# Optimization experiments

Measured on AMD Instinct MI355X. Metric: run time of the kernel, lower is better.

## Reference

```python
import jax, jax.numpy as jnp
import numpy as np
import math

B, SQ, SK, HEADS, DH = 4, 4096, 308, 8, 64
INNER = HEADS * DH


def setup_inputs() -> dict:
    key = jax.random.key(0)
    k1, k2, k3, k4, k5 = jax.random.split(key, 5)
    q = jax.random.normal(k1, (B, SQ, INNER), dtype=jnp.float32)
    k = jax.random.normal(k2, (B, SK, INNER), dtype=jnp.float32)
    v = jax.random.normal(k3, (B, SK, INNER), dtype=jnp.float32)
    # mask_scale: positive multiplicative rescale (H*W / mask_area in original)
    mask_scale = jax.random.uniform(k4, (B, HEADS, SQ, SK), dtype=jnp.float32) + 0.5
    # mask_bool: region membership mask (masks > 0.5 in original)
    mask_bool = jax.random.randint(k5, (B, HEADS, SQ, SK), 0, 2) > 0
    return {"q": q, "k": k, "v": v, "mask_scale": mask_scale,
            "mask_bool": mask_bool, "heads": HEADS}


def reference(q, k, v, mask_scale, mask_bool, heads):
    b, sq, inner = q.shape
    dh = inner // heads
    # (b, s, h*dh) -> (b, h, s, dh)
    def split_heads(t):
        return t.reshape(b, -1, heads, dh).transpose(0, 2, 1, 3)
    qh, kh, vh = split_heads(q), split_heads(k), split_heads(v)
    scores = jnp.einsum('bhqd,bhkd->bhqk', qh, kh) / math.sqrt(dh)
    scores = scores * mask_scale
    scores = jnp.where(mask_bool, scores, -jnp.inf)
    attn = jax.nn.softmax(scores, axis=-1)
    out = jnp.einsum('bhqk,bhkd->bhqd', attn, vh)
    # (b, h, q, dh) -> (b, q, h*dh)
    return out.transpose(0, 2, 1, 3).reshape(b, sq, heads * dh)
```

## Files before the change

### kernel.cpp

```cpp
#include <hip/hip_runtime.h>


#define NB     4
#define NSQ    4096
#define NSK    308
#define NH     8
#define NDH    64
#define NINNER 512
#define NKT    20
#define QTILE  128
#define NTHREADS 512
#define PF     4
#define LDS_BYTES ((NKT*2*64*8 + NKT*4*64*4) * 2)

typedef _Float16 h8 __attribute__((ext_vector_type(8)));
typedef _Float16 h4 __attribute__((ext_vector_type(4)));
typedef float    f4 __attribute__((ext_vector_type(4)));
typedef int      i4 __attribute__((ext_vector_type(4)));

__global__ __launch_bounds__(NTHREADS) void omost_attn(
    const float* __restrict__ Qg, const float* __restrict__ Kg,
    const float* __restrict__ Vg, const float* __restrict__ MSg,
    const int*   __restrict__ MBg, float* __restrict__ Og)
{
  extern __shared__ __align__(16) _Float16 smem[];
  _Float16* Klds = smem;
  _Float16* Vlds = smem + NKT*2*64*8;

  const int tid  = threadIdx.x;
  const int lane = tid & 63;
  const int wv   = tid >> 6;
  const int lg   = lane >> 4;
  const int lr   = lane & 15;

  const int wg = blockIdx.x;
  const int qt = wg & (NSQ / QTILE - 1);
  const int bh = wg >> 5;
  const int b  = bh >> 3;
  const int h  = bh & 7;

  const int q0   = qt * QTILE + wv * 16;
  const int qrow = q0 + lr;
  const size_t mrow = ((size_t)bh * NSQ + qrow) * NSK;

  f4 msb[PF];
  i4 mbb[PF];
  #pragma unroll
  for (int d = 0; d < PF; ++d) {
    int kb = d * 16 + lg * 4;
    msb[d] = *(const f4*)(MSg + mrow + kb);
    mbb[d] = *(const i4*)(MBg + mrow + kb);
  }

  const float* Kb = Kg + (size_t)b * NSK * NINNER + h * NDH;
  #pragma unroll
  for (int i = 0; i < (NKT*2*64) / NTHREADS; ++i) {
    int s   = tid + i * NTHREADS;
    int l   = s & 63;
    int dhc = (s >> 6) & 1;
    int kt  = s >> 7;
    int row = kt * 16 + (l & 15);
    int col = dhc * 32 + ((l >> 4) << 3);
    h8 hk;
    #pragma unroll
    for (int j = 0; j < 8; ++j) hk[j] = (_Float16)0.f;
    if (row < NSK) {
      const float* p = Kb + (size_t)row * NINNER + col;
      f4 a = *(const f4*)p;
      f4 c = *(const f4*)(p + 4);
      hk[0]=(_Float16)a[0]; hk[1]=(_Float16)a[1]; hk[2]=(_Float16)a[2]; hk[3]=(_Float16)a[3];
      hk[4]=(_Float16)c[0]; hk[5]=(_Float16)c[1]; hk[6]=(_Float16)c[2]; hk[7]=(_Float16)c[3];
    }
    *(h8*)(Klds + (size_t)s * 8) = hk;
  }

  const float* Vb = Vg + (size_t)b * NSK * NINNER + h * NDH;
  #pragma unroll
  for (int i = 0; i < (NKT*4*64) / NTHREADS; ++i) {
    int s    = tid + i * NTHREADS;
    int l    = s & 63;
    int nt   = (s >> 6) & 3;
    int kt   = s >> 8;
    int col  = nt * 16 + (l & 15);
    int row0 = kt * 16 + ((l >> 4) << 2);
    h4 hv;
    #pragma unroll
    for (int j = 0; j < 4; ++j) hv[j] = (_Float16)0.f;
    #pragma unroll
    for (int j = 0; j < 4; ++j) {
      int row = row0 + j;
      if (row < NSK) hv[j] = (_Float16)Vb[(size_t)row * NINNER + col];
    }
    *(h4*)(Vlds + (size_t)s * 4) = hv;
  }
  __syncthreads();

  const float NEG_INF = -__builtin_inff();

  const float* Qb = Qg + ((size_t)b * NSQ + qrow) * NINNER + h * NDH;
  h8 qf[2];
  #pragma unroll
  for (int dhc = 0; dhc < 2; ++dhc) {
    const float* p = Qb + dhc * 32 + lg * 8;
    f4 a = *(const f4*)p;
    f4 c = *(const f4*)(p + 4);
    h8 t;
    t[0]=(_Float16)a[0]; t[1]=(_Float16)a[1]; t[2]=(_Float16)a[2]; t[3]=(_Float16)a[3];
    t[4]=(_Float16)c[0]; t[5]=(_Float16)c[1]; t[6]=(_Float16)c[2]; t[7]=(_Float16)c[3];
    qf[dhc] = t;
  }

  f4 S[NKT];
  float rmax = NEG_INF;
  const h8* Kf = (const h8*)Klds;
  #pragma unroll
  for (int kt = 0; kt < NKT; ++kt) {
    f4 ms = msb[kt % PF];
    i4 mb = mbb[kt % PF];
    if (kt + PF < NKT) {
      int kb  = (kt + PF) * 16 + lg * 4;
      int kbl = kb > (NSK - 4) ? (NSK - 4) : kb;
      msb[(kt + PF) % PF] = *(const f4*)(MSg + mrow + kbl);
      mbb[(kt + PF) % PF] = *(const i4*)(MBg + mrow + kbl);
    }
    f4 c = {0.f, 0.f, 0.f, 0.f};
    c = __builtin_amdgcn_mfma_f32_16x16x32_f16(Kf[(kt*2+0)*64 + lane], qf[0], c, 0, 0, 0);
    c = __builtin_amdgcn_mfma_f32_16x16x32_f16(Kf[(kt*2+1)*64 + lane], qf[1], c, 0, 0, 0);

    const int kb0 = kt * 16 + lg * 4;
    f4 s;
    #pragma unroll
    for (int r = 0; r < 4; ++r) {
      bool ok = (kb0 + r < NSK) && (mb[r] != 0);
      s[r] = ok ? c[r] * 0.125f * ms[r] : NEG_INF;
      rmax = fmaxf(rmax, s[r]);
    }
    S[kt] = s;
  }

  rmax = fmaxf(rmax, __shfl_xor(rmax, 16, 64));
  rmax = fmaxf(rmax, __shfl_xor(rmax, 32, 64));
  float ssum = 0.f;
  #pragma unroll
  for (int kt = 0; kt < NKT; ++kt) {
    f4 s = S[kt];
    #pragma unroll
    for (int r = 0; r < 4; ++r) { float p = __expf(s[r] - rmax); s[r] = p; ssum += p; }
    S[kt] = s;
  }
  ssum += __shfl_xor(ssum, 16, 64);
  ssum += __shfl_xor(ssum, 32, 64);
  const float inv = 1.f / ssum;

  f4 acc[4];
  #pragma unroll
  for (int nt = 0; nt < 4; ++nt) acc[nt] = (f4){0.f, 0.f, 0.f, 0.f};
  const h4* Vf = (const h4*)Vlds;
  #pragma unroll
  for (int kt = 0; kt < NKT; ++kt) {
    h4 pa;
    #pragma unroll
    for (int r = 0; r < 4; ++r) pa[r] = (_Float16)(S[kt][r] * inv);
    #pragma unroll
    for (int nt = 0; nt < 4; ++nt)
      acc[nt] = __builtin_amdgcn_mfma_f32_16x16x16f16(pa, Vf[(kt*4+nt)*64 + lane], acc[nt], 0, 0, 0);
  }

  float* Ob = Og + (size_t)b * NSQ * NINNER + h * NDH;
  #pragma unroll
  for (int nt = 0; nt < 4; ++nt) {
    #pragma unroll
    for (int r = 0; r < 4; ++r) {
      int qq = q0 + lg * 4 + r;
      Ob[(size_t)qq * NINNER + nt * 16 + lr] = acc[nt][r];
    }
  }
}

extern "C" void kernel_launch(void* const* d_in, const int* in_sizes, int n_in,
                              void* d_out, int out_size, void* d_ws, size_t ws_size,
                              hipStream_t stream) {
  const float* Qg  = (const float*)d_in[0];
  const float* Kg  = (const float*)d_in[1];
  const float* Vg  = (const float*)d_in[2];
  const float* MSg = (const float*)d_in[3];
  const int*   MBg = (const int*)d_in[4];
  float* Og = (float*)d_out;

  static_assert(LDS_BYTES <= 160 * 1024, "exceeds gfx950 LDS");
  (void)hipFuncSetAttribute((const void*)omost_attn,
                            hipFuncAttributeMaxDynamicSharedMemorySize, LDS_BYTES);

  const int nwg = NB * NH * (NSQ / QTILE);
  omost_attn<<<dim3(nwg), dim3(NTHREADS), LDS_BYTES, stream>>>(Qg, Kg, Vg, MSg, MBg, Og);
}
```

Measured before the change: 112.4 us.

## Precompute K/V fp16 MFMA fragments in a prep kernel, read from global workspace

K and V are converted to fp16 MFMA fragment layout once per (batch, head) in a separate prep kernel and stored in the workspace. The attention kernel no longer stages them in LDS; it reads fragments straight from global memory, where they should mostly hit in L2. Block size drops to 256 threads with 64-query tiles, doubling the workgroup count. This removes the per-workgroup K/V conversion, the LDS staging and the barrier, and frees LDS for occupancy. In exchange it adds a second launch and relies on cache hits for repeated fragment reads. The launch returns silently if the workspace is too small.

```diff
diff --git a/kernel.cpp b/kernel.cpp
--- a/kernel.cpp
+++ b/kernel.cpp
@@ -8,54 +8,34 @@
 #define NDH    64
 #define NINNER 512
 #define NKT    20
-#define QTILE  128
-#define NTHREADS 512
+#define NTHREADS 256
 #define PF     4
-#define LDS_BYTES ((NKT*2*64*8 + NKT*4*64*4) * 2)
+
+#define KFRAG_PER_BH (NKT*2*64*8)
+#define VFRAG_PER_BH (NKT*4*64*4)
+#define WS_BYTES ((size_t)(NB*NH) * (KFRAG_PER_BH + VFRAG_PER_BH) * 2)
 
 typedef _Float16 h8 __attribute__((ext_vector_type(8)));
 typedef _Float16 h4 __attribute__((ext_vector_type(4)));
 typedef float    f4 __attribute__((ext_vector_type(4)));
 typedef int      i4 __attribute__((ext_vector_type(4)));
 
-__global__ __launch_bounds__(NTHREADS) void omost_attn(
-    const float* __restrict__ Qg, const float* __restrict__ Kg,
-    const float* __restrict__ Vg, const float* __restrict__ MSg,
-    const int*   __restrict__ MBg, float* __restrict__ Og)
+__global__ __launch_bounds__(512) void omost_prep(
+    const float* __restrict__ Kg, const float* __restrict__ Vg,
+    _Float16* __restrict__ ws)
 {
-  extern __shared__ __align__(16) _Float16 smem[];
-  _Float16* Klds = smem;
-  _Float16* Vlds = smem + NKT*2*64*8;
-
-  const int tid  = threadIdx.x;
-  const int lane = tid & 63;
-  const int wv   = tid >> 6;
-  const int lg   = lane >> 4;
-  const int lr   = lane & 15;
-
-  const int wg = blockIdx.x;
-  const int qt = wg & (NSQ / QTILE - 1);
-  const int bh = wg >> 5;
-  const int b  = bh >> 3;
-  const int h  = bh & 7;
-
-  const int q0   = qt * QTILE + wv * 16;
-  const int qrow = q0 + lr;
-  const size_t mrow = ((size_t)bh * NSQ + qrow) * NSK;
-
-  f4 msb[PF];
-  i4 mbb[PF];
-  #pragma unroll
-  for (int d = 0; d < PF; ++d) {
-    int kb = d * 16 + lg * 4;
-    msb[d] = *(const f4*)(MSg + mrow + kb);
-    mbb[d] = *(const i4*)(MBg + mrow + kb);
-  }
+  const int bh  = blockIdx.x;
+  const int b   = bh >> 3;
+  const int h   = bh & 7;
+  const int tid = threadIdx.x;
+
+  _Float16* Kfrag = ws + (size_t)bh * KFRAG_PER_BH;
+  _Float16* Vfrag = ws + (size_t)(NB*NH) * KFRAG_PER_BH + (size_t)bh * VFRAG_PER_BH;
 
   const float* Kb = Kg + (size_t)b * NSK * NINNER + h * NDH;
   #pragma unroll
-  for (int i = 0; i < (NKT*2*64) / NTHREADS; ++i) {
-    int s   = tid + i * NTHREADS;
+  for (int i = 0; i < (NKT*2*64) / 512; ++i) {
+    int s   = tid + i * 512;
     int l   = s & 63;
     int dhc = (s >> 6) & 1;
     int kt  = s >> 7;
@@ -71,13 +51,13 @@
       hk[0]=(_Float16)a[0]; hk[1]=(_Float16)a[1]; hk[2]=(_Float16)a[2]; hk[3]=(_Float16)a[3];
       hk[4]=(_Float16)c[0]; hk[5]=(_Float16)c[1]; hk[6]=(_Float16)c[2]; hk[7]=(_Float16)c[3];
     }
-    *(h8*)(Klds + (size_t)s * 8) = hk;
+    *(h8*)(Kfrag + (size_t)s * 8) = hk;
   }
 
   const float* Vb = Vg + (size_t)b * NSK * NINNER + h * NDH;
   #pragma unroll
-  for (int i = 0; i < (NKT*4*64) / NTHREADS; ++i) {
-    int s    = tid + i * NTHREADS;
+  for (int i = 0; i < (NKT*4*64) / 512; ++i) {
+    int s    = tid + i * 512;
     int l    = s & 63;
     int nt   = (s >> 6) & 3;
     int kt   = s >> 8;
@@ -91,9 +71,42 @@
       int row = row0 + j;
       if (row < NSK) hv[j] = (_Float16)Vb[(size_t)row * NINNER + col];
     }
-    *(h4*)(Vlds + (size_t)s * 4) = hv;
-  }
-  __syncthreads();
+    *(h4*)(Vfrag + (size_t)s * 4) = hv;
+  }
+}
+
+__global__ __launch_bounds__(NTHREADS) void omost_attn(
+    const float* __restrict__ Qg, const float* __restrict__ MSg,
+    const int*   __restrict__ MBg, const _Float16* __restrict__ ws,
+    float* __restrict__ Og)
+{
+  const int tid  = threadIdx.x;
+  const int lane = tid & 63;
+  const int wv   = tid >> 6;
+  const int lg   = lane >> 4;
+  const int lr   = lane & 15;
+
+  const int wg = blockIdx.x;
+  const int qt = wg & (NSQ / 64 - 1);
+  const int bh = wg >> 6;
+  const int b  = bh >> 3;
+  const int h  = bh & 7;
+
+  const int q0   = qt * 64 + wv * 16;
+  const int qrow = q0 + lr;
+  const size_t mrow = ((size_t)bh * NSQ + qrow) * NSK;
+
+  const h8* Kf = (const h8*)(ws + (size_t)bh * KFRAG_PER_BH);
+  const h4* Vf = (const h4*)(ws + (size_t)(NB*NH) * KFRAG_PER_BH + (size_t)bh * VFRAG_PER_BH);
+
+  f4 msb[PF];
+  i4 mbb[PF];
+  #pragma unroll
+  for (int d = 0; d < PF; ++d) {
+    int kb = d * 16 + lg * 4;
+    msb[d] = *(const f4*)(MSg + mrow + kb);
+    mbb[d] = *(const i4*)(MBg + mrow + kb);
+  }
 
   const float NEG_INF = -__builtin_inff();
 
@@ -112,7 +125,6 @@
 
   f4 S[NKT];
   float rmax = NEG_INF;
-  const h8* Kf = (const h8*)Klds;
   #pragma unroll
   for (int kt = 0; kt < NKT; ++kt) {
     f4 ms = msb[kt % PF];
@@ -155,7 +167,6 @@
   f4 acc[4];
   #pragma unroll
   for (int nt = 0; nt < 4; ++nt) acc[nt] = (f4){0.f, 0.f, 0.f, 0.f};
-  const h4* Vf = (const h4*)Vlds;
   #pragma unroll
   for (int kt = 0; kt < NKT; ++kt) {
     h4 pa;
@@ -186,11 +197,12 @@
   const float* MSg = (const float*)d_in[3];
   const int*   MBg = (const int*)d_in[4];
   float* Og = (float*)d_out;
-
-  static_assert(LDS_BYTES <= 160 * 1024, "exceeds gfx950 LDS");
-  (void)hipFuncSetAttribute((const void*)omost_attn,
-                            hipFuncAttributeMaxDynamicSharedMemorySize, LDS_BYTES);
-
-  const int nwg = NB * NH * (NSQ / QTILE);
-  omost_attn<<<dim3(nwg), dim3(NTHREADS), LDS_BYTES, stream>>>(Qg, Kg, Vg, MSg, MBg, Og);
+  _Float16* ws = (_Float16*)d_ws;
+
+  if (ws_size < WS_BYTES) return;
+
+  omost_prep<<<dim3(NB*NH), dim3(512), 0, stream>>>(Kg, Vg, ws);
+
+  const int nwg = NB * NH * (NSQ / 64);
+  omost_attn<<<dim3(nwg), dim3(NTHREADS), 0, stream>>>(Qg, MSg, MBg, ws, Og);
 }
```

Result: slower. 119.7 us (+6.5%).
